# Kernel optimization log

Hardware: AMD Instinct MI355X
Metric: run time of the kernel (lower is better)

The kernel has to match this reference:

```python
import jax, jax.numpy as jnp
import numpy as np

B, E, L, D = 16, 256, 4096, 512

def setup_inputs() -> dict:
    key = jax.random.key(0)
    k1, k2, k3 = jax.random.split(key, 3)
    doc_state = jax.random.normal(k1, (B, L, D), dtype=jnp.float32)
    # soft membership weights (original multiplies then sums over L)
    entity_mapping = jax.random.uniform(k2, (B, E, L), dtype=jnp.float32)
    # positive span lengths for the division
    entity_lens = jax.random.uniform(k3, (B, E), dtype=jnp.float32) * 100.0 + 1.0
    return {"doc_state": doc_state, "entity_mapping": entity_mapping, "entity_lens": entity_lens}

def reference(doc_state, entity_mapping, entity_lens):
    # sum_L(mapping[b,e,l] * doc[b,l,d]) == batched matmul; avoids (B,E,L,D) blow-up
    pooled = jnp.einsum('bel,bld->bed', entity_mapping, doc_state)  # (B,E,D)
    return pooled / entity_lens[:, :, None]
```

## Files before the change

kernel.cpp:

```cpp
#include <hip/hip_runtime.h>
#include <hip/hip_bf16.h>


#define NB 16
#define NE 256
#define NL 4096
#define ND 512
#define KSPLIT 4
#define KPW (NL / KSPLIT)
#define BK 32
#define NT (KPW / BK)

using f32x4  = __attribute__((ext_vector_type(4))) float;
using u32x2  = __attribute__((ext_vector_type(2))) unsigned;
using u32x4  = __attribute__((ext_vector_type(4))) unsigned;
using bf16x8 = __attribute__((ext_vector_type(8))) short;

static __device__ __forceinline__ unsigned bfbits(float x) {
  return (unsigned)__builtin_bit_cast(unsigned short, (__bf16)x);
}
static __device__ __forceinline__ unsigned lds_u32(const void* p) {
  return (unsigned)(size_t)(const __attribute__((address_space(3))) void*)p;
}

#define GLOADX4(DST, PTR) \
  asm volatile("global_load_dwordx4 %0, %1, off" : "=v"(DST) : "v"(PTR))
#define DSW64(ADDR, D, OFF) \
  asm volatile("ds_write_b64 %0, %1 offset:" OFF :: "v"(ADDR), "v"(D) : "memory")
#define DSW128(ADDR, D, OFF) \
  asm volatile("ds_write_b128 %0, %1 offset:" OFF :: "v"(ADDR), "v"(D) : "memory")
#define DSR128(DST, ADDR, OFF) \
  asm volatile("ds_read_b128 %0, %1 offset:" OFF : "=v"(DST) : "v"(ADDR))
#define WAIT_VM(N)  asm volatile("s_waitcnt vmcnt(" #N ")" ::: "memory")
#define WAIT_LGKM() asm volatile("s_waitcnt lgkmcnt(0)" ::: "memory")
#define SB0()       __builtin_amdgcn_sched_barrier(0)

#define STAGE_ISSUE(RS, T)                                                     \
  do {                                                                         \
    const float* p_ = gthr + (size_t)(T) * tstep;                              \
    GLOADX4(RS[0], p_ + st0[0]); GLOADX4(RS[1], p_ + st0[1]);                  \
    GLOADX4(RS[2], p_ + st0[2]); GLOADX4(RS[3], p_ + st0[3]);                  \
    GLOADX4(RS[4], p_ + st0[4]); GLOADX4(RS[5], p_ + st0[5]);                  \
    GLOADX4(RS[6], p_ + st0[6]); GLOADX4(RS[7], p_ + st0[7]);                  \
  } while (0)

#define STAGE_WRITE(RS, OFFS)                                                  \
  do {                                                                         \
    if (isB) {                                                                 \
      _Pragma("unroll") for (int j_ = 0; j_ < 4; ++j_) {                       \
        u32x4 wv_;                                                             \
        _Pragma("unroll") for (int k_ = 0; k_ < 4; ++k_)                       \
            wv_[k_] = bfbits(RS[2 * k_][j_]) | (bfbits(RS[2 * k_ + 1][j_]) << 16); \
        DSW128(wAddr[j_], wv_, OFFS);                                          \
      }                                                                        \
    } else {                                                                   \
      _Pragma("unroll") for (int i_ = 0; i_ < 8; ++i_) {                       \
        u32x2 wv_;                                                             \
        wv_[0] = bfbits(RS[i_][0]) | (bfbits(RS[i_][1]) << 16);                \
        wv_[1] = bfbits(RS[i_][2]) | (bfbits(RS[i_][3]) << 16);                \
        DSW64(wAddr[i_], wv_, OFFS);                                           \
      }                                                                        \
    }                                                                          \
  } while (0)

#define COMPUTE(OFFS)                                                          \
  do {                                                                         \
    bf16x8 af_[4], bf_[4];                                                     \
    DSR128(af_[0], aRd[0], OFFS); DSR128(af_[1], aRd[1], OFFS);                \
    DSR128(af_[2], aRd[2], OFFS); DSR128(af_[3], aRd[3], OFFS);                \
    DSR128(bf_[0], bRd[0], OFFS); DSR128(bf_[1], bRd[1], OFFS);                \
    DSR128(bf_[2], bRd[2], OFFS); DSR128(bf_[3], bRd[3], OFFS);                \
    WAIT_LGKM();                                                               \
    SB0();                                                                     \
    __builtin_amdgcn_s_setprio(1);                                             \
    _Pragma("unroll") for (int m_ = 0; m_ < 4; ++m_)                           \
        _Pragma("unroll") for (int n_ = 0; n_ < 4; ++n_)                       \
            acc[m_][n_] = __builtin_amdgcn_mfma_f32_16x16x32_bf16(             \
                af_[m_], bf_[n_], acc[m_][n_], 0, 0, 0);                       \
    __builtin_amdgcn_s_setprio(0);                                             \
    SB0();                                                                     \
  } while (0)

__global__ __launch_bounds__(256, 2) void mp_gemm(const float* __restrict__ doc,
                                                  const float* __restrict__ emap,
                                                  const float* __restrict__ lens,
                                                  float* __restrict__ out) {
  __shared__ char smem[2 * 16384];

  int bid = (int)blockIdx.x;
  int logical = (bid & 7) * 64 + (bid >> 3);
  int b    = logical >> 5;
  int rest = logical & 31;
  int et = rest >> 4;
  int dt = (rest >> 2) & 3;
  int ks = rest & 3;

  int tid  = (int)threadIdx.x;
  int w    = tid >> 6;
  int wr   = w >> 1;
  int wc   = w & 1;
  int lane = tid & 63;
  int l15  = lane & 15;
  int g    = lane >> 4;

  unsigned ldsb = lds_u32(smem);
  bool isB = (tid < 128);

  const float* gthr;
  size_t tstep = (size_t)BK;
  int st0[8];
  unsigned wAddr[8];

  if (isB) {
    int q = tid & 31, o = tid >> 5;
    gthr = doc + ((size_t)b * NL + ks * KPW + 8 * o) * ND + dt * 128 + 4 * q;
    tstep = (size_t)BK * ND;
#pragma unroll
    for (int i = 0; i < 8; ++i) st0[i] = i * ND;
#pragma unroll
    for (int j = 0; j < 4; ++j)
      wAddr[j] = ldsb + 8192 + (4 * q + j) * 64 + (((o ^ q) & 3) << 4);
  } else {
    int v = tid - 128;
    int rowb = v >> 2, ch = v & 3;
    gthr = emap + (size_t)(b * NE + et * 128 + rowb) * NL + ks * KPW + 4 * ch;
    tstep = (size_t)BK;
#pragma unroll
    for (int r = 0; r < 4; ++r)
#pragma unroll
      for (int h = 0; h < 2; ++h) st0[2 * r + h] = r * 32 * NL + h * 16;
#pragma unroll
    for (int r = 0; r < 4; ++r)
#pragma unroll
      for (int h = 0; h < 2; ++h) {
        int row = 32 * r + rowb;
        int c16 = 2 * h + (ch >> 1);
        wAddr[2 * r + h] = ldsb + row * 64 + (((c16 ^ row) & 3) << 4) + (ch & 1) * 8;
      }
  }

  unsigned aRd[4], bRd[4];
#pragma unroll
  for (int m = 0; m < 4; ++m) {
    int row = 64 * wr + 16 * m + l15;
    aRd[m] = ldsb + row * 64 + (((g ^ row) & 3) << 4);
  }
#pragma unroll
  for (int n = 0; n < 4; ++n) {
    int d = 64 * wc + 16 * n + l15;
    bRd[n] = ldsb + 8192 + d * 64 + (((g ^ (d >> 2)) & 3) << 4);
  }

  f32x4 acc[4][4] = {};
  f32x4 RS0[8], RS1[8];

  STAGE_ISSUE(RS0, 0);
  SB0();
  STAGE_ISSUE(RS1, 1);
  SB0();
  WAIT_VM(8);
  SB0();
  STAGE_WRITE(RS0, "0");

#pragma unroll 1
  for (int t = 0; t < NT; t += 2) {
    int p2 = t + 2 < NT ? t + 2 : NT - 1;
    int p3 = t + 3 < NT ? t + 3 : NT - 1;
    WAIT_LGKM();
    __builtin_amdgcn_s_barrier();
    SB0();
    STAGE_ISSUE(RS0, p2);
    SB0();
    COMPUTE("0");
    WAIT_VM(8);
    SB0();
    STAGE_WRITE(RS1, "16384");
    WAIT_LGKM();
    __builtin_amdgcn_s_barrier();
    SB0();
    STAGE_ISSUE(RS1, p3);
    SB0();
    COMPUTE("16384");
    WAIT_VM(8);
    SB0();
    STAGE_WRITE(RS0, "0");
  }

  WAIT_VM(0);
  SB0();

  const float* lb = lens + b * NE + et * 128 + 64 * wr;
  float* ob = out + (size_t)(b * NE + et * 128 + 64 * wr) * ND + dt * 128 + 64 * wc;
#pragma unroll
  for (int m = 0; m < 4; ++m) {
#pragma unroll
    for (int i = 0; i < 4; ++i) {
      int row = 16 * m + 4 * g + i;
      float inv = 1.0f / lb[row];
#pragma unroll
      for (int n = 0; n < 4; ++n)
        unsafeAtomicAdd(&ob[(size_t)row * ND + 16 * n + l15], acc[m][n][i] * inv);
    }
  }
}

extern "C" void kernel_launch(void* const* d_in, const int* in_sizes, int n_in,
                              void* d_out, int out_size, void* d_ws, size_t ws_size,
                              hipStream_t stream) {
  const float* doc  = (const float*)d_in[0];
  const float* emap = (const float*)d_in[1];
  const float* lens = (const float*)d_in[2];
  float* out = (float*)d_out;
  hipMemsetAsync(out, 0, (size_t)NB * NE * ND * sizeof(float), stream);
  hipLaunchKernelGGL(mp_gemm, dim3(512), dim3(256), 0, stream, doc, emap, lens, out);
}
```

Baseline: 63.91 us.

## Enlarge block tile to 256x256 with 8-way K split and single register stage

Each block now covers all 256 entities and 256 of the D columns with 512 threads and 8 waves, each wave holding an 8x4 grid of MFMA accumulators. K is split 8 ways instead of 4, and the grid shrinks to 256 blocks. The prefetch drops from two register stages to one with full vmcnt(0) waits, so each global load is exposed before its LDS write. The aim is more reuse of every loaded tile and fewer reloads of the mapping and doc data, at the cost of more atomic output traffic, higher register pressure, and weaker latency hiding.

```diff
diff --git a/kernel.cpp b/kernel.cpp
--- a/kernel.cpp
+++ b/kernel.cpp
@@ -6,7 +6,7 @@
 #define NE 256
 #define NL 4096
 #define ND 512
-#define KSPLIT 4
+#define KSPLIT 8
 #define KPW (NL / KSPLIT)
 #define BK 32
 #define NT (KPW / BK)
@@ -31,7 +31,7 @@
   asm volatile("ds_write_b128 %0, %1 offset:" OFF :: "v"(ADDR), "v"(D) : "memory")
 #define DSR128(DST, ADDR, OFF) \
   asm volatile("ds_read_b128 %0, %1 offset:" OFF : "=v"(DST) : "v"(ADDR))
-#define WAIT_VM(N)  asm volatile("s_waitcnt vmcnt(" #N ")" ::: "memory")
+#define WAIT_VM0()  asm volatile("s_waitcnt vmcnt(0)" ::: "memory")
 #define WAIT_LGKM() asm volatile("s_waitcnt lgkmcnt(0)" ::: "memory")
 #define SB0()       __builtin_amdgcn_sched_barrier(0)
 
@@ -63,17 +63,19 @@
     }                                                                          \
   } while (0)
 
-#define COMPUTE(OFFS)                                                          \
+#define COMPUTE(AB, BB)                                                        \
   do {                                                                         \
-    bf16x8 af_[4], bf_[4];                                                     \
-    DSR128(af_[0], aRd[0], OFFS); DSR128(af_[1], aRd[1], OFFS);                \
-    DSR128(af_[2], aRd[2], OFFS); DSR128(af_[3], aRd[3], OFFS);                \
-    DSR128(bf_[0], bRd[0], OFFS); DSR128(bf_[1], bRd[1], OFFS);                \
-    DSR128(bf_[2], bRd[2], OFFS); DSR128(bf_[3], bRd[3], OFFS);                \
+    bf16x8 af_[8], bf_[4];                                                     \
+    DSR128(af_[0], AB, "0");    DSR128(af_[1], AB, "1024");                    \
+    DSR128(af_[2], AB, "2048"); DSR128(af_[3], AB, "3072");                    \
+    DSR128(af_[4], AB, "4096"); DSR128(af_[5], AB, "5120");                    \
+    DSR128(af_[6], AB, "6144"); DSR128(af_[7], AB, "7168");                    \
+    DSR128(bf_[0], BB, "0");    DSR128(bf_[1], BB, "1024");                    \
+    DSR128(bf_[2], BB, "2048"); DSR128(bf_[3], BB, "3072");                    \
     WAIT_LGKM();                                                               \
     SB0();                                                                     \
     __builtin_amdgcn_s_setprio(1);                                             \
-    _Pragma("unroll") for (int m_ = 0; m_ < 4; ++m_)                           \
+    _Pragma("unroll") for (int m_ = 0; m_ < 8; ++m_)                           \
         _Pragma("unroll") for (int n_ = 0; n_ < 4; ++n_)                       \
             acc[m_][n_] = __builtin_amdgcn_mfma_f32_16x16x32_bf16(             \
                 af_[m_], bf_[n_], acc[m_][n_], 0, 0, 0);                       \
@@ -81,118 +83,101 @@
     SB0();                                                                     \
   } while (0)
 
-__global__ __launch_bounds__(256, 2) void mp_gemm(const float* __restrict__ doc,
+__global__ __launch_bounds__(512, 2) void mp_gemm(const float* __restrict__ doc,
                                                   const float* __restrict__ emap,
                                                   const float* __restrict__ lens,
                                                   float* __restrict__ out) {
-  __shared__ char smem[2 * 16384];
+  __shared__ char smem[2 * 32768];
 
   int bid = (int)blockIdx.x;
-  int logical = (bid & 7) * 64 + (bid >> 3);
-  int b    = logical >> 5;
-  int rest = logical & 31;
-  int et = rest >> 4;
-  int dt = (rest >> 2) & 3;
-  int ks = rest & 3;
+  int logical = (bid & 7) * 32 + (bid >> 3);
+  int b  = logical >> 4;
+  int dt = (logical >> 3) & 1;
+  int ks = logical & 7;
 
   int tid  = (int)threadIdx.x;
   int w    = tid >> 6;
-  int wr   = w >> 1;
-  int wc   = w & 1;
+  int wr   = w >> 2;
+  int wc   = w & 3;
   int lane = tid & 63;
   int l15  = lane & 15;
   int g    = lane >> 4;
 
   unsigned ldsb = lds_u32(smem);
-  bool isB = (tid < 128);
+  bool isB = (tid < 256);
 
   const float* gthr;
-  size_t tstep = (size_t)BK;
+  size_t tstep;
   int st0[8];
   unsigned wAddr[8];
 
   if (isB) {
-    int q = tid & 31, o = tid >> 5;
-    gthr = doc + ((size_t)b * NL + ks * KPW + 8 * o) * ND + dt * 128 + 4 * q;
+    int q = tid & 63, o = w;
+    gthr = doc + ((size_t)b * NL + ks * KPW + 8 * o) * ND + dt * 256 + 4 * q;
     tstep = (size_t)BK * ND;
 #pragma unroll
     for (int i = 0; i < 8; ++i) st0[i] = i * ND;
 #pragma unroll
     for (int j = 0; j < 4; ++j)
-      wAddr[j] = ldsb + 8192 + (4 * q + j) * 64 + (((o ^ q) & 3) << 4);
+      wAddr[j] = ldsb + 16384 + (4 * q + j) * 64 + (((o ^ q) & 3) << 4);
   } else {
-    int v = tid - 128;
-    int rowb = v >> 2, ch = v & 3;
-    gthr = emap + (size_t)(b * NE + et * 128 + rowb) * NL + ks * KPW + 4 * ch;
+    int v = tid - 256;
+    int rowb = v >> 3, c = v & 7;
+    gthr = emap + (size_t)(b * NE + rowb) * NL + ks * KPW + 4 * c;
     tstep = (size_t)BK;
 #pragma unroll
-    for (int r = 0; r < 4; ++r)
-#pragma unroll
-      for (int h = 0; h < 2; ++h) st0[2 * r + h] = r * 32 * NL + h * 16;
-#pragma unroll
-    for (int r = 0; r < 4; ++r)
-#pragma unroll
-      for (int h = 0; h < 2; ++h) {
-        int row = 32 * r + rowb;
-        int c16 = 2 * h + (ch >> 1);
-        wAddr[2 * r + h] = ldsb + row * 64 + (((c16 ^ row) & 3) << 4) + (ch & 1) * 8;
-      }
+    for (int i = 0; i < 8; ++i) st0[i] = i * 32 * NL;
+#pragma unroll
+    for (int i = 0; i < 8; ++i) {
+      int r = rowb + 32 * i;
+      wAddr[i] = ldsb + r * 64 + ((((c >> 1) ^ r) & 3) << 4) + (c & 1) * 8;
+    }
   }
 
-  unsigned aRd[4], bRd[4];
-#pragma unroll
-  for (int m = 0; m < 4; ++m) {
-    int row = 64 * wr + 16 * m + l15;
-    aRd[m] = ldsb + row * 64 + (((g ^ row) & 3) << 4);
-  }
-#pragma unroll
-  for (int n = 0; n < 4; ++n) {
-    int d = 64 * wc + 16 * n + l15;
-    bRd[n] = ldsb + 8192 + d * 64 + (((g ^ (d >> 2)) & 3) << 4);
-  }
-
-  f32x4 acc[4][4] = {};
-  f32x4 RS0[8], RS1[8];
-
-  STAGE_ISSUE(RS0, 0);
+  unsigned aRd0 = ldsb + (128 * wr + l15) * 64 + (((g ^ l15) & 3) << 4);
+  unsigned aRd1 = aRd0 + 32768;
+  unsigned bRd0 = ldsb + 16384 + (64 * wc + l15) * 64 + (((g ^ (l15 >> 2)) & 3) << 4);
+  unsigned bRd1 = bRd0 + 32768;
+
+  f32x4 acc[8][4] = {};
+  f32x4 RS[8];
+
+  STAGE_ISSUE(RS, 0);
   SB0();
-  STAGE_ISSUE(RS1, 1);
+  WAIT_VM0();
   SB0();
-  WAIT_VM(8);
-  SB0();
-  STAGE_WRITE(RS0, "0");
+  STAGE_WRITE(RS, "0");
+  WAIT_LGKM();
 
 #pragma unroll 1
   for (int t = 0; t < NT; t += 2) {
     int p2 = t + 2 < NT ? t + 2 : NT - 1;
-    int p3 = t + 3 < NT ? t + 3 : NT - 1;
+    __builtin_amdgcn_s_barrier();
+    SB0();
+    STAGE_ISSUE(RS, t + 1);
+    SB0();
+    COMPUTE(aRd0, bRd0);
+    WAIT_VM0();
+    SB0();
+    STAGE_WRITE(RS, "32768");
     WAIT_LGKM();
+    SB0();
     __builtin_amdgcn_s_barrier();
     SB0();
-    STAGE_ISSUE(RS0, p2);
-    SB0();
-    COMPUTE("0");
-    WAIT_VM(8);
-    SB0();
-    STAGE_WRITE(RS1, "16384");
+    STAGE_ISSUE(RS, p2);
+    SB0();
+    COMPUTE(aRd1, bRd1);
+    WAIT_VM0();
+    SB0();
+    STAGE_WRITE(RS, "0");
     WAIT_LGKM();
-    __builtin_amdgcn_s_barrier();
-    SB0();
-    STAGE_ISSUE(RS1, p3);
-    SB0();
-    COMPUTE("16384");
-    WAIT_VM(8);
-    SB0();
-    STAGE_WRITE(RS0, "0");
+    SB0();
   }
 
-  WAIT_VM(0);
-  SB0();
-
-  const float* lb = lens + b * NE + et * 128 + 64 * wr;
-  float* ob = out + (size_t)(b * NE + et * 128 + 64 * wr) * ND + dt * 128 + 64 * wc;
-#pragma unroll
-  for (int m = 0; m < 4; ++m) {
+  const float* lb = lens + b * NE + 128 * wr;
+  float* ob = out + (size_t)(b * NE + 128 * wr) * ND + dt * 256 + 64 * wc;
+#pragma unroll
+  for (int m = 0; m < 8; ++m) {
 #pragma unroll
     for (int i = 0; i < 4; ++i) {
       int row = 16 * m + 4 * g + i;
@@ -212,5 +197,5 @@
   const float* lens = (const float*)d_in[2];
   float* out = (float*)d_out;
   hipMemsetAsync(out, 0, (size_t)NB * NE * ND * sizeof(float), stream);
-  hipLaunchKernelGGL(mp_gemm, dim3(512), dim3(256), 0, stream, doc, emap, lens, out);
-}
+  hipLaunchKernelGGL(mp_gemm, dim3(256), dim3(512), 0, stream, doc, emap, lens, out);
+}
```

Measured after the change: 89.12 us. +39.5%, slower.
